# Performance work log

Measured on AMD Instinct MI355X. Metric: run time of the kernel, lower is better.

Reference implementation:

```python
import jax, jax.numpy as jnp
import numpy as np

GRID_SIZE = 5
SPLINE_ORDER = 3
NUM_BASIS = GRID_SIZE + SPLINE_ORDER  # 8


def make_grid():
    # knots: grid_size + 2*spline_order + 1 = 12 points over extended [-1,1]
    h = 2.0 / GRID_SIZE
    return (jnp.arange(-SPLINE_ORDER, GRID_SIZE + SPLINE_ORDER + 1, dtype=jnp.float32) * h - 1.0)[None, :]  # (1, 12)


def b_splines(x, grid):
    # x: (N, in) -> bases: (N, in, NUM_BASIS) via Cox-de Boor recursion
    x = x[..., None]  # (N, in, 1)
    bases = ((x >= grid[:, :-1]) & (x < grid[:, 1:])).astype(x.dtype)
    for p in range(1, SPLINE_ORDER + 1):
        left = (x - grid[:, : -(p + 1)]) / (grid[:, p:-1] - grid[:, : -(p + 1)])
        right = (grid[:, p + 1:] - x) / (grid[:, p + 1:] - grid[:, 1:-p])
        bases = left * bases[..., :-1] + right * bases[..., 1:]
    return bases


def kan_linear(x, base_w, spline_w, scaler, grid):
    # x: (N, in); base_w: (out, in); spline_w: (out, in, G); scaler: (out, in)
    base = jnp.einsum('ni,oi->no', jax.nn.silu(x), base_w)
    bases = b_splines(x, grid)  # (N, in, G)
    spline = jnp.einsum('nig,oig->no', bases, spline_w * scaler[..., None])
    return base + spline


def setup_inputs() -> dict:
    key = jax.random.key(0)
    ks = jax.random.split(key, 7)
    H, L = 768, 2
    hidden = jax.random.normal(ks[0], (32, 512, H), dtype=jnp.float32)
    s = 0.1
    return {
        'hidden': hidden,
        'base_w1': jax.random.normal(ks[1], (H, H), jnp.float32) * s,
        'spline_w1': jax.random.normal(ks[2], (H, H, NUM_BASIS), jnp.float32) * s,
        'scaler1': jax.random.normal(ks[3], (H, H), jnp.float32) * s + 1.0,
        'base_w2': jax.random.normal(ks[4], (L, H), jnp.float32) * s,
        'spline_w2': jax.random.normal(ks[5], (L, H, NUM_BASIS), jnp.float32) * s,
        'scaler2': jax.random.normal(ks[6], (L, H), jnp.float32) * s + 1.0,
    }


def reference(hidden, base_w1, spline_w1, scaler1, base_w2, spline_w2, scaler2):
    grid = make_grid()
    B, S, H = hidden.shape
    x = hidden.reshape(-1, H)  # (N, H)
    x = kan_linear(x, base_w1, spline_w1, scaler1, grid)
    x = jax.nn.gelu(x, approximate=False)  # torch F.gelu default = erf
    out = kan_linear(x, base_w2, spline_w2, scaler2, grid)  # (N, L)
    return out.reshape(B, S, -1).squeeze(-1) if out.shape[-1] == 1 else out.reshape(B, S, -1)
```

## Files before the change

kernel.cpp:

```cpp
#include <hip/hip_runtime.h>
#include <math.h>

#define NROWS 16384
#define H     768
#define KEXP  6912
#define NCHUNK 108
#define NITER 54

typedef __attribute__((ext_vector_type(8))) short  bhalf8;
typedef __attribute__((ext_vector_type(4))) float  floatx4;

__device__ __forceinline__ unsigned short f2bf(float f) {
    unsigned int u = __float_as_uint(f);
    u = (u + 0x7FFFu + ((u >> 16) & 1u)) >> 16;
    return (unsigned short)u;
}
__device__ __forceinline__ float bf2f(unsigned short h) {
    return __uint_as_float(((unsigned int)h) << 16);
}
__device__ __forceinline__ unsigned int pack2(unsigned short a, unsigned short b) {
    return (unsigned int)a | ((unsigned int)b << 16);
}
__device__ __forceinline__ float silu_f(float x) { return x / (1.0f + __expf(-x)); }

__device__ __forceinline__ float gelu_fast(float x) {
    float x3 = x * x * x;
    float y = fmaf(x3, 0.0356774081f, x * 0.7978845608f);
    float e = __expf(2.0f * y);
    float th = 1.0f - 2.0f / (e + 1.0f);
    return 0.5f * x * (1.0f + th);
}

__device__ __forceinline__ void kan_bases(float x, float* __restrict__ b) {
    const float c6 = 0.166666666667f;
    float u  = fmaf(x, 2.5f, 5.5f);
    float fj = floorf(u);
    float t  = u - fj;
    int  j0  = (int)fj;
    float t2 = t * t, t3 = t2 * t;
    float n0 = t3 * c6;
    float n1 = fmaf(t3, -0.5f, fmaf(t2, 0.5f, fmaf(t, 0.5f, c6)));
    float n2 = fmaf(t3, 0.5f, fmaf(t2, -1.0f, 0.666666666667f));
    float omt = 1.0f - t;
    float n3 = omt * omt * omt * c6;
#pragma unroll
    for (int c = 0; c < 8; ++c) {
        int d = j0 - c;
        float v = (d == 0) ? n0 : 0.0f;
        v = (d == 1) ? n1 : v;
        v = (d == 2) ? n2 : v;
        v = (d == 3) ? n3 : v;
        b[c] = v;
    }
}

__global__ __launch_bounds__(256) void prep_expand(
    const float* __restrict__ x, const float* __restrict__ bw,
    const float* __restrict__ sw, const float* __restrict__ sc,
    unsigned short* __restrict__ wp, unsigned short* __restrict__ F)
{
    const int b = blockIdx.x, t = threadIdx.x;
    if (b < H) {
        const int n = b;
        const float* bwr = bw + (size_t)n * H;
        unsigned short* out = wp + (size_t)n * KEXP;
        if (t < 96) {
            const float4* xp = (const float4*)(bwr + t * 8);
            float4 v0 = xp[0], v1 = xp[1];
            uint4 pk;
            pk.x = pack2(f2bf(v0.x), f2bf(v0.y));
            pk.y = pack2(f2bf(v0.z), f2bf(v0.w));
            pk.z = pack2(f2bf(v1.x), f2bf(v1.y));
            pk.w = pack2(f2bf(v1.z), f2bf(v1.w));
            *(uint4*)(out + t * 8) = pk;
        }
#pragma unroll
        for (int p = 0; p < 3; ++p) {
            int i = t + p * 256;
            float s = sc[(size_t)n * H + i];
            const float4* swp = (const float4*)(sw + ((size_t)n * H + i) * 8);
            float4 w0 = swp[0], w1 = swp[1];
            uint4 pk;
            pk.x = pack2(f2bf(w0.x * s), f2bf(w0.y * s));
            pk.y = pack2(f2bf(w0.z * s), f2bf(w0.w * s));
            pk.z = pack2(f2bf(w1.x * s), f2bf(w1.y * s));
            pk.w = pack2(f2bf(w1.z * s), f2bf(w1.w * s));
            *(uint4*)(out + H + (size_t)i * 8) = pk;
        }
    } else {
        const int n = b - H;
        __shared__ float sX[H];
        const float* xr = x + (size_t)n * H;
        if (t < 192) ((float4*)sX)[t] = ((const float4*)xr)[t];
        __syncthreads();
        unsigned short* out = F + (size_t)n * KEXP;
        if (t < 96) {
            const float4* xp = (const float4*)(sX + t * 8);
            float4 v0 = xp[0], v1 = xp[1];
            uint4 pk;
            pk.x = pack2(f2bf(silu_f(v0.x)), f2bf(silu_f(v0.y)));
            pk.y = pack2(f2bf(silu_f(v0.z)), f2bf(silu_f(v0.w)));
            pk.z = pack2(f2bf(silu_f(v1.x)), f2bf(silu_f(v1.y)));
            pk.w = pack2(f2bf(silu_f(v1.z)), f2bf(silu_f(v1.w)));
            *(uint4*)(out + t * 8) = pk;
        }
#pragma unroll
        for (int p = 0; p < 3; ++p) {
            int i = t + p * 256;
            float xv = sX[i];
            float bb[8];
            kan_bases(xv, bb);
            uint4 pk;
            pk.x = pack2(f2bf(bb[0]), f2bf(bb[1]));
            pk.y = pack2(f2bf(bb[2]), f2bf(bb[3]));
            pk.z = pack2(f2bf(bb[4]), f2bf(bb[5]));
            pk.w = pack2(f2bf(bb[6]), f2bf(bb[7]));
            *(uint4*)(out + H + (size_t)i * 8) = pk;
        }
    }
}


#define AS1 __attribute__((address_space(1)))
#define AS3 __attribute__((address_space(3)))

#define DSR(D, A, O) asm volatile("ds_read_b128 %0, %1 offset:" #O : "=v"(D) : "v"(A) : "memory")
#define LDA(O) do{ DSR(fA[0],avA[0],O); DSR(fA[1],avA[1],O); DSR(fA[2],avA[2],O); DSR(fA[3],avA[3],O); \
                   DSR(fA[4],avA[4],O); DSR(fA[5],avA[5],O); DSR(fA[6],avA[6],O); DSR(fA[7],avA[7],O); }while(0)
#define LDB(O) do{ DSR(fB[0],avB[0],O); DSR(fB[1],avB[1],O); DSR(fB[2],avB[2],O); DSR(fB[3],avB[3],O); }while(0)

#define MM(QM,QN) do{ \
    _Pragma("unroll") \
    for (int kk = 0; kk < 2; ++kk) \
        _Pragma("unroll") \
        for (int im = 0; im < 4; ++im) \
            _Pragma("unroll") \
            for (int in_ = 0; in_ < 2; ++in_) \
                acc[QM][QN][im][in_] = __builtin_amdgcn_mfma_f32_16x16x32_bf16( \
                    fA[im*2+kk], fB[in_*2+kk], acc[QM][QN][im][in_], 0, 0, 0); \
}while(0)

#define STG_A(BF,HH,KS) do{ \
    __builtin_amdgcn_global_load_lds((const AS1 void*)(pA##HH[0] + (size_t)(KS)*64), \
        (AS3 void*)&sA[BF][HH][wb8], 16, 0, 0); \
    __builtin_amdgcn_global_load_lds((const AS1 void*)(pA##HH[1] + (size_t)(KS)*64), \
        (AS3 void*)&sA[BF][HH][4096 + wb8], 16, 0, 0); \
}while(0)
#define STG_B(BF,HH,KS) do{ \
    __builtin_amdgcn_global_load_lds((const AS1 void*)(pB##HH[0] + (size_t)(KS)*64), \
        (AS3 void*)&sB[BF][HH][wb8], 16, 0, 0); \
    __builtin_amdgcn_global_load_lds((const AS1 void*)(pB##HH[1] + (size_t)(KS)*64), \
        (AS3 void*)&sB[BF][HH][4096 + wb8], 16, 0, 0); \
}while(0)

#define PH_MID do{ __builtin_amdgcn_s_barrier(); \
    asm volatile("s_waitcnt lgkmcnt(0)" ::: "memory"); \
    __builtin_amdgcn_sched_barrier(0); \
    __builtin_amdgcn_s_setprio(1); }while(0)
#define PH_END do{ __builtin_amdgcn_s_setprio(0); \
    __builtin_amdgcn_sched_barrier(0); \
    __builtin_amdgcn_s_barrier(); }while(0)
#define PH_END_VMN(N) do{ __builtin_amdgcn_s_setprio(0); \
    __builtin_amdgcn_sched_barrier(0); \
    asm volatile("s_waitcnt vmcnt(" #N ")" ::: "memory"); \
    __builtin_amdgcn_s_barrier(); }while(0)

__global__ __launch_bounds__(512, 2) void kan1_gemm(
    const unsigned short* __restrict__ F, const unsigned short* __restrict__ wp,
    unsigned short* __restrict__ l1)
{
    __shared__ __align__(16) unsigned short sA[2][2][8192];
    __shared__ __align__(16) unsigned short sB[2][2][8192];

    const int b = blockIdx.x;
    const int swz = (b & 7) * 24 + (b >> 3);
    const int rowT = swz / 3, colT = swz - rowT * 3;
    const int rowBase = rowT * 256, colBase = colT * 256;

    const int t = threadIdx.x;
    const int lane = t & 63;
    const int quad = lane >> 4, lm = lane & 15, p7 = lane & 7;
    const int wv = t >> 6, wr = wv & 1, wc = wv >> 1;

    const int rr = t >> 3;
    const int slotx = (t & 7) ^ (rr & 7);
    const int wb8 = (t & 448) * 8;

    const unsigned short* pA0[2]; const unsigned short* pA1[2];
    const unsigned short* pB0[2]; const unsigned short* pB1[2];
#pragma unroll
    for (int p = 0; p < 2; ++p) {
        pA0[p] = F  + (size_t)(rowBase +       p*64 + rr) * KEXP + slotx*8;
        pA1[p] = F  + (size_t)(rowBase + 128 + p*64 + rr) * KEXP + slotx*8;
        pB0[p] = wp + (size_t)(colBase +       p*64 + rr) * KEXP + slotx*8;
        pB1[p] = wp + (size_t)(colBase + 128 + p*64 + rr) * KEXP + slotx*8;
    }

    unsigned int avA[8], avB[4];
    {
        unsigned int aB = (unsigned int)(size_t)(AS3 unsigned short*)&sA[0][0][0];
        unsigned int bB = (unsigned int)(size_t)(AS3 unsigned short*)&sB[0][0][0];
#pragma unroll
        for (int im = 0; im < 4; ++im)
#pragma unroll
            for (int kk = 0; kk < 2; ++kk)
                avA[im*2+kk] = aB + (unsigned)(((wr*64 + im*16 + lm)*64 + (((kk*4+quad)^p7)*8)) * 2);
#pragma unroll
        for (int in_ = 0; in_ < 2; ++in_)
#pragma unroll
            for (int kk = 0; kk < 2; ++kk)
                avB[in_*2+kk] = bB + (unsigned)(((wc*32 + in_*16 + lm)*64 + (((kk*4+quad)^p7)*8)) * 2);
    }

    floatx4 acc[2][2][4][2] = {};
    bhalf8 fA[8], fB[4];

    STG_A(0,0,0); STG_A(0,1,0); STG_B(0,0,0); STG_B(0,1,0);
    STG_B(1,0,1); STG_A(1,1,1);
    asm volatile("s_waitcnt vmcnt(4)" ::: "memory");
    __builtin_amdgcn_s_barrier();

#pragma unroll 1
    for (int i = 0; i < NITER - 1; ++i) {
        const int b1 = 2*i + 1, nx = 2*i + 2, nb = 2*i + 3;
        LDA(0);     LDB(0);     STG_A(1,0,b1); PH_MID; MM(0,0); PH_END;
        LDA(16384);             STG_B(1,1,b1); PH_MID; MM(1,0); PH_END;
        LDB(16384);             STG_B(0,0,nx); PH_MID; MM(1,1); PH_END;
        LDA(0);                 STG_A(0,1,nx); PH_MID; MM(0,1); PH_END_VMN(4);
        LDA(32768); LDB(32768); STG_A(0,0,nx); PH_MID; MM(0,0); PH_END;
        LDA(49152);             STG_B(0,1,nx); PH_MID; MM(1,0); PH_END;
        LDB(49152);             STG_B(1,0,nb); PH_MID; MM(1,1); PH_END;
        LDA(32768);             STG_A(1,1,nb); PH_MID; MM(0,1); PH_END_VMN(4);
    }
    LDA(0);     LDB(0);     STG_A(1,0,107); PH_MID; MM(0,0); PH_END;
    LDA(16384);             STG_B(1,1,107); PH_MID; MM(1,0); PH_END;
    LDB(16384);                             PH_MID; MM(1,1); PH_END;
    LDA(0);                                 PH_MID; MM(0,1); PH_END_VMN(0);
    LDA(32768); LDB(32768);                 PH_MID; MM(0,0); PH_END;
    LDA(49152);                             PH_MID; MM(1,0); PH_END;
    LDB(49152);                             PH_MID; MM(1,1); PH_END;
    LDA(32768);                             PH_MID; MM(0,1); PH_END;

#pragma unroll
    for (int qm = 0; qm < 2; ++qm)
#pragma unroll
    for (int qn = 0; qn < 2; ++qn)
#pragma unroll
    for (int im = 0; im < 4; ++im)
#pragma unroll
    for (int in_ = 0; in_ < 2; ++in_) {
        const int row0 = rowBase + qm*128 + wr*64 + im*16 + quad*4;
        const int col  = colBase + qn*128 + wc*32 + in_*16 + lm;
#pragma unroll
        for (int rg = 0; rg < 4; ++rg)
            l1[(size_t)(row0 + rg) * H + col] = f2bf(acc[qm][qn][im][in_][rg]);
    }
}

__global__ __launch_bounds__(256) void kan2_kernel(
    const unsigned short* __restrict__ l1, const float* __restrict__ bw,
    const float* __restrict__ sw, const float* __restrict__ sc,
    float* __restrict__ out)
{
    const int lane = threadIdx.x & 63;
    const int wv = threadIdx.x >> 6;
    const int n = blockIdx.x * 4 + wv;
    float a0 = 0.f, a1 = 0.f;
#pragma unroll
    for (int ii = 0; ii < H / 64; ++ii) {
        int i = lane + ii * 64;
        float h = bf2f(l1[(size_t)n * H + i]);
        float u = gelu_fast(h);
        float f0 = silu_f(u);
        float bb[8];
        kan_bases(u, bb);
        float bw0 = bw[i], bw1 = bw[H + i];
        float s0 = sc[i], s1 = sc[H + i];
        const float4* q0 = (const float4*)(sw + (size_t)i * 8);
        const float4* q1 = (const float4*)(sw + (size_t)(H + i) * 8);
        float4 w00 = q0[0], w01 = q0[1];
        float4 w10 = q1[0], w11 = q1[1];
        float t0 = bb[0]*w00.x + bb[1]*w00.y + bb[2]*w00.z + bb[3]*w00.w
                 + bb[4]*w01.x + bb[5]*w01.y + bb[6]*w01.z + bb[7]*w01.w;
        float t1 = bb[0]*w10.x + bb[1]*w10.y + bb[2]*w10.z + bb[3]*w10.w
                 + bb[4]*w11.x + bb[5]*w11.y + bb[6]*w11.z + bb[7]*w11.w;
        a0 += f0 * bw0 + s0 * t0;
        a1 += f0 * bw1 + s1 * t1;
    }
#pragma unroll
    for (int off = 32; off > 0; off >>= 1) {
        a0 += __shfl_down(a0, off, 64);
        a1 += __shfl_down(a1, off, 64);
    }
    if (lane == 0) {
        out[(size_t)n * 2 + 0] = a0;
        out[(size_t)n * 2 + 1] = a1;
    }
}

extern "C" void kernel_launch(void* const* d_in, const int* in_sizes, int n_in,
                              void* d_out, int out_size, void* d_ws, size_t ws_size,
                              hipStream_t stream) {
    const float* hidden = (const float*)d_in[0];
    const float* bw1    = (const float*)d_in[1];
    const float* sw1    = (const float*)d_in[2];
    const float* sc1    = (const float*)d_in[3];
    const float* bw2    = (const float*)d_in[4];
    const float* sw2    = (const float*)d_in[5];
    const float* sc2    = (const float*)d_in[6];
    float* out = (float*)d_out;

    const size_t l1_elems = (size_t)NROWS * H;
    const size_t wp_elems = (size_t)H * KEXP;
    unsigned short* l1 = (unsigned short*)d_ws;
    unsigned short* wp = l1 + l1_elems;
    unsigned short* F  = wp + wp_elems;

    prep_expand<<<H + NROWS, 256, 0, stream>>>(hidden, bw1, sw1, sc1, wp, F);
    kan1_gemm<<<192, 512, 0, stream>>>(F, wp, l1);
    kan2_kernel<<<NROWS / 4, 256, 0, stream>>>(l1, bw2, sw2, sc2, out);
}
```

Measured before the change: 355.4 us.

## Retile KAN GEMM to 256x192 tiles with 256 blocks and new pipeline

The main GEMM moves from 256x256 output tiles on 192 blocks to 256x192 tiles on 256 blocks, so every CU on the MI355X gets a block and the last wave is less uneven. The B operand now lives in three 64-row LDS slabs. The phase schedule is rewritten with separate A fragment registers for the two row halves, new prefetch ordering and vmcnt waits, and the loop tail is folded into the main loop by clamping the K indices. In exchange, each tile has a lower compute-to-load ratio and the tail redundantly reloads the last chunk, and the new waitcnt choreography carries a correctness risk.

```diff
diff --git a/kernel.cpp b/kernel.cpp
--- a/kernel.cpp
+++ b/kernel.cpp
@@ -125,19 +125,27 @@
 #define AS3 __attribute__((address_space(3)))
 
 #define DSR(D, A, O) asm volatile("ds_read_b128 %0, %1 offset:" #O : "=v"(D) : "v"(A) : "memory")
-#define LDA(O) do{ DSR(fA[0],avA[0],O); DSR(fA[1],avA[1],O); DSR(fA[2],avA[2],O); DSR(fA[3],avA[3],O); \
-                   DSR(fA[4],avA[4],O); DSR(fA[5],avA[5],O); DSR(fA[6],avA[6],O); DSR(fA[7],avA[7],O); }while(0)
-#define LDB(O) do{ DSR(fB[0],avB[0],O); DSR(fB[1],avB[1],O); DSR(fB[2],avB[2],O); DSR(fB[3],avB[3],O); }while(0)
-
-#define MM(QM,QN) do{ \
+#define LDA0(O) do{ DSR(fA0[0],avA[0],O); DSR(fA0[1],avA[1],O); DSR(fA0[2],avA[2],O); DSR(fA0[3],avA[3],O); \
+                    DSR(fA0[4],avA[4],O); DSR(fA0[5],avA[5],O); DSR(fA0[6],avA[6],O); DSR(fA0[7],avA[7],O); }while(0)
+#define LDA1(O) do{ DSR(fA1[0],avA[0],O); DSR(fA1[1],avA[1],O); DSR(fA1[2],avA[2],O); DSR(fA1[3],avA[3],O); \
+                    DSR(fA1[4],avA[4],O); DSR(fA1[5],avA[5],O); DSR(fA1[6],avA[6],O); DSR(fA1[7],avA[7],O); }while(0)
+#define LDB(O)  do{ DSR(fB[0],avB[0],O); DSR(fB[1],avB[1],O); }while(0)
+
+#define MM0(QN) do{ \
     _Pragma("unroll") \
     for (int kk = 0; kk < 2; ++kk) \
         _Pragma("unroll") \
         for (int im = 0; im < 4; ++im) \
-            _Pragma("unroll") \
-            for (int in_ = 0; in_ < 2; ++in_) \
-                acc[QM][QN][im][in_] = __builtin_amdgcn_mfma_f32_16x16x32_bf16( \
-                    fA[im*2+kk], fB[in_*2+kk], acc[QM][QN][im][in_], 0, 0, 0); \
+            acc0[QN][im] = __builtin_amdgcn_mfma_f32_16x16x32_bf16( \
+                fA0[im*2+kk], fB[kk], acc0[QN][im], 0, 0, 0); \
+}while(0)
+#define MM1(QN) do{ \
+    _Pragma("unroll") \
+    for (int kk = 0; kk < 2; ++kk) \
+        _Pragma("unroll") \
+        for (int im = 0; im < 4; ++im) \
+            acc1[QN][im] = __builtin_amdgcn_mfma_f32_16x16x32_bf16( \
+                fA1[im*2+kk], fB[kk], acc1[QN][im], 0, 0, 0); \
 }while(0)
 
 #define STG_A(BF,HH,KS) do{ \
@@ -146,12 +154,9 @@
     __builtin_amdgcn_global_load_lds((const AS1 void*)(pA##HH[1] + (size_t)(KS)*64), \
         (AS3 void*)&sA[BF][HH][4096 + wb8], 16, 0, 0); \
 }while(0)
-#define STG_B(BF,HH,KS) do{ \
-    __builtin_amdgcn_global_load_lds((const AS1 void*)(pB##HH[0] + (size_t)(KS)*64), \
-        (AS3 void*)&sB[BF][HH][wb8], 16, 0, 0); \
-    __builtin_amdgcn_global_load_lds((const AS1 void*)(pB##HH[1] + (size_t)(KS)*64), \
-        (AS3 void*)&sB[BF][HH][4096 + wb8], 16, 0, 0); \
-}while(0)
+#define STG_B(BF,QN,KS) \
+    __builtin_amdgcn_global_load_lds((const AS1 void*)(pB[QN] + (size_t)(KS)*64), \
+        (AS3 void*)&sB[BF][QN][wb8], 16, 0, 0)
 
 #define PH_MID do{ __builtin_amdgcn_s_barrier(); \
     asm volatile("s_waitcnt lgkmcnt(0)" ::: "memory"); \
@@ -170,12 +175,13 @@
     unsigned short* __restrict__ l1)
 {
     __shared__ __align__(16) unsigned short sA[2][2][8192];
-    __shared__ __align__(16) unsigned short sB[2][2][8192];
+    __shared__ __align__(16) unsigned short sB[2][3][4096];
 
     const int b = blockIdx.x;
-    const int swz = (b & 7) * 24 + (b >> 3);
-    const int rowT = swz / 3, colT = swz - rowT * 3;
-    const int rowBase = rowT * 256, colBase = colT * 256;
+    const int s = b >> 3;
+    const int rowT = (b & 7) * 8 + (s >> 2);
+    const int colT = s & 3;
+    const int rowBase = rowT * 256, colBase = colT * 192;
 
     const int t = threadIdx.x;
     const int lane = t & 63;
@@ -187,16 +193,17 @@
     const int wb8 = (t & 448) * 8;
 
     const unsigned short* pA0[2]; const unsigned short* pA1[2];
-    const unsigned short* pB0[2]; const unsigned short* pB1[2];
+    const unsigned short* pB[3];
 #pragma unroll
     for (int p = 0; p < 2; ++p) {
-        pA0[p] = F  + (size_t)(rowBase +       p*64 + rr) * KEXP + slotx*8;
-        pA1[p] = F  + (size_t)(rowBase + 128 + p*64 + rr) * KEXP + slotx*8;
-        pB0[p] = wp + (size_t)(colBase +       p*64 + rr) * KEXP + slotx*8;
-        pB1[p] = wp + (size_t)(colBase + 128 + p*64 + rr) * KEXP + slotx*8;
-    }
-
-    unsigned int avA[8], avB[4];
+        pA0[p] = F + (size_t)(rowBase +       p*64 + rr) * KEXP + slotx*8;
+        pA1[p] = F + (size_t)(rowBase + 128 + p*64 + rr) * KEXP + slotx*8;
+    }
+#pragma unroll
+    for (int q = 0; q < 3; ++q)
+        pB[q] = wp + (size_t)(colBase + q*64 + rr) * KEXP + slotx*8;
+
+    unsigned int avA[8], avB[2];
     {
         unsigned int aB = (unsigned int)(size_t)(AS3 unsigned short*)&sA[0][0][0];
         unsigned int bB = (unsigned int)(size_t)(AS3 unsigned short*)&sB[0][0][0];
@@ -206,54 +213,51 @@
             for (int kk = 0; kk < 2; ++kk)
                 avA[im*2+kk] = aB + (unsigned)(((wr*64 + im*16 + lm)*64 + (((kk*4+quad)^p7)*8)) * 2);
 #pragma unroll
-        for (int in_ = 0; in_ < 2; ++in_)
-#pragma unroll
-            for (int kk = 0; kk < 2; ++kk)
-                avB[in_*2+kk] = bB + (unsigned)(((wc*32 + in_*16 + lm)*64 + (((kk*4+quad)^p7)*8)) * 2);
-    }
-
-    floatx4 acc[2][2][4][2] = {};
-    bhalf8 fA[8], fB[4];
-
-    STG_A(0,0,0); STG_A(0,1,0); STG_B(0,0,0); STG_B(0,1,0);
-    STG_B(1,0,1); STG_A(1,1,1);
-    asm volatile("s_waitcnt vmcnt(4)" ::: "memory");
+        for (int kk = 0; kk < 2; ++kk)
+            avB[kk] = bB + (unsigned)(((wc*16 + lm)*64 + (((kk*4+quad)^p7)*8)) * 2);
+    }
+
+    floatx4 acc0[3][4] = {};
+    floatx4 acc1[3][4] = {};
+    bhalf8 fA0[8], fA1[8], fB[2];
+
+    STG_A(0,0,0); STG_A(0,1,0); STG_B(0,0,0); STG_B(0,1,0); STG_B(0,2,0);
+    STG_A(1,0,1); STG_A(1,1,1); STG_B(1,0,1); STG_B(1,1,1);
+    asm volatile("s_waitcnt vmcnt(8)" ::: "memory");
     __builtin_amdgcn_s_barrier();
 
 #pragma unroll 1
-    for (int i = 0; i < NITER - 1; ++i) {
-        const int b1 = 2*i + 1, nx = 2*i + 2, nb = 2*i + 3;
-        LDA(0);     LDB(0);     STG_A(1,0,b1); PH_MID; MM(0,0); PH_END;
-        LDA(16384);             STG_B(1,1,b1); PH_MID; MM(1,0); PH_END;
-        LDB(16384);             STG_B(0,0,nx); PH_MID; MM(1,1); PH_END;
-        LDA(0);                 STG_A(0,1,nx); PH_MID; MM(0,1); PH_END_VMN(4);
-        LDA(32768); LDB(32768); STG_A(0,0,nx); PH_MID; MM(0,0); PH_END;
-        LDA(49152);             STG_B(0,1,nx); PH_MID; MM(1,0); PH_END;
-        LDB(49152);             STG_B(1,0,nb); PH_MID; MM(1,1); PH_END;
-        LDA(32768);             STG_A(1,1,nb); PH_MID; MM(0,1); PH_END_VMN(4);
-    }
-    LDA(0);     LDB(0);     STG_A(1,0,107); PH_MID; MM(0,0); PH_END;
-    LDA(16384);             STG_B(1,1,107); PH_MID; MM(1,0); PH_END;
-    LDB(16384);                             PH_MID; MM(1,1); PH_END;
-    LDA(0);                                 PH_MID; MM(0,1); PH_END_VMN(0);
-    LDA(32768); LDB(32768);                 PH_MID; MM(0,0); PH_END;
-    LDA(49152);                             PH_MID; MM(1,0); PH_END;
-    LDB(49152);                             PH_MID; MM(1,1); PH_END;
-    LDA(32768);                             PH_MID; MM(0,1); PH_END;
-
-#pragma unroll
-    for (int qm = 0; qm < 2; ++qm)
-#pragma unroll
-    for (int qn = 0; qn < 2; ++qn)
-#pragma unroll
-    for (int im = 0; im < 4; ++im)
-#pragma unroll
-    for (int in_ = 0; in_ < 2; ++in_) {
-        const int row0 = rowBase + qm*128 + wr*64 + im*16 + quad*4;
-        const int col  = colBase + qn*128 + wc*32 + in_*16 + lm;
-#pragma unroll
-        for (int rg = 0; rg < 4; ++rg)
-            l1[(size_t)(row0 + rg) * H + col] = f2bf(acc[qm][qn][im][in_][rg]);
+    for (int i = 0; i < NITER; ++i) {
+        const int k1 = 2*i + 1;
+        const int k2 = (2*i + 2 > 107) ? 107 : 2*i + 2;
+        const int k3 = (2*i + 3 > 107) ? 107 : 2*i + 3;
+        LDA0(0);     LDB(0);     STG_B(1,2,k1);               PH_MID; MM0(0);         PH_END_VMN(10);
+        LDA1(16384);             STG_A(0,0,k2);               PH_MID; MM1(0);         PH_END_VMN(10);
+        LDB(8192);               STG_A(0,1,k2);               PH_MID; MM1(1); MM0(1); PH_END_VMN(11);
+        LDB(16384);              STG_B(0,0,k2); STG_B(0,1,k2);PH_MID; MM0(2); MM1(2); PH_END_VMN(8);
+        LDA0(32768); LDB(24576); STG_B(0,2,k2);               PH_MID; MM0(0);         PH_END;
+        LDA1(49152);             STG_A(1,0,k3);               PH_MID; MM1(0);         PH_END_VMN(10);
+        LDB(32768);              STG_A(1,1,k3);               PH_MID; MM1(1); MM0(1); PH_END_VMN(11);
+        LDB(40960);              STG_B(1,0,k3); STG_B(1,1,k3);PH_MID; MM0(2); MM1(2); PH_END_VMN(8);
+    }
+
+#pragma unroll
+    for (int qn = 0; qn < 3; ++qn)
+#pragma unroll
+    for (int im = 0; im < 4; ++im) {
+        const int col = colBase + qn*64 + wc*16 + lm;
+        {
+            const int row0 = rowBase + wr*64 + im*16 + quad*4;
+#pragma unroll
+            for (int rg = 0; rg < 4; ++rg)
+                l1[(size_t)(row0 + rg) * H + col] = f2bf(acc0[qn][im][rg]);
+        }
+        {
+            const int row0 = rowBase + 128 + wr*64 + im*16 + quad*4;
+#pragma unroll
+            for (int rg = 0; rg < 4; ++rg)
+                l1[(size_t)(row0 + rg) * H + col] = f2bf(acc1[qn][im][rg]);
+        }
     }
 }
 
@@ -317,6 +321,6 @@
     unsigned short* F  = wp + wp_elems;
 
     prep_expand<<<H + NROWS, 256, 0, stream>>>(hidden, bw1, sw1, sc1, wp, F);
-    kan1_gemm<<<192, 512, 0, stream>>>(F, wp, l1);
+    kan1_gemm<<<256, 512, 0, stream>>>(F, wp, l1);
     kan2_kernel<<<NROWS / 4, 256, 0, stream>>>(l1, bw2, sw2, sc2, out);
 }
```

After: 336.4 us. 1.06x faster.
